# Performance work log

Measured on AMD Instinct MI355X. Metric: run time of the kernel, lower is better.

The kernel has to match this reference:

```python
import jax, jax.numpy as jnp
import numpy as np

N_NODES = 100000
N_EDGES = 1600000
IN_F = 67
H1, C1 = 10, 8   # heads, per-head channels layer 1
H2, C2 = 1, 1    # layer 2


def setup_inputs() -> dict:
    key = jax.random.key(0)
    ks = jax.random.split(key, 10)
    x = jax.random.normal(ks[0], (N_NODES, IN_F), dtype=jnp.float32)
    edge_index = jax.random.randint(ks[1], (2, N_EDGES), 0, N_NODES, dtype=jnp.int64)
    s = 0.1
    W1 = jax.random.normal(ks[2], (IN_F, H1 * C1), dtype=jnp.float32) * s
    att_src1 = jax.random.normal(ks[3], (H1, C1), dtype=jnp.float32) * s
    att_dst1 = jax.random.normal(ks[4], (H1, C1), dtype=jnp.float32) * s
    b1 = jnp.zeros((H1 * C1,), dtype=jnp.float32)
    W2 = jax.random.normal(ks[5], (H1 * C1, H2 * C2), dtype=jnp.float32) * s
    att_src2 = jax.random.normal(ks[6], (H2, C2), dtype=jnp.float32) * s
    att_dst2 = jax.random.normal(ks[7], (H2, C2), dtype=jnp.float32) * s
    b2 = jnp.zeros((H2 * C2,), dtype=jnp.float32)
    return {"x": x, "edge_index": edge_index, "W1": W1, "att_src1": att_src1,
            "att_dst1": att_dst1, "b1": b1, "W2": W2, "att_src2": att_src2,
            "att_dst2": att_dst2, "b2": b2}


def gat_conv(x, src, dst, W, att_src, att_dst, bias, heads, out_ch):
    """PyG GATConv (eval mode): gather -> leaky_relu -> segment softmax -> scatter."""
    n = x.shape[0]
    h = (x @ W).reshape(n, heads, out_ch)                     # [N,H,C]
    a_src = jnp.sum(h * att_src, axis=-1)                     # [N,H]
    a_dst = jnp.sum(h * att_dst, axis=-1)                     # [N,H]
    e = a_src[src] + a_dst[dst]                               # [E,H]
    e = jax.nn.leaky_relu(e, negative_slope=0.2)
    # numerically stable softmax over edges grouped by destination node
    m = jax.ops.segment_max(e, dst, num_segments=n)           # [N,H]
    ex = jnp.exp(e - m[dst])
    denom = jax.ops.segment_sum(ex, dst, num_segments=n)      # [N,H]
    alpha = ex / denom[dst]                                   # [E,H]
    msg = h[src] * alpha[:, :, None]                          # [E,H,C]
    out = jax.ops.segment_sum(msg, dst, num_segments=n)       # [N,H,C]
    return out.reshape(n, heads * out_ch) + bias


def reference(x, edge_index, W1, att_src1, att_dst1, b1, W2, att_src2, att_dst2, b2):
    n = x.shape[0]
    loops = jnp.arange(n, dtype=edge_index.dtype)
    src = jnp.concatenate([edge_index[0], loops])             # add_self_loops=True
    dst = jnp.concatenate([edge_index[1], loops])
    h = gat_conv(x, src, dst, W1, att_src1, att_dst1, b1, H1, C1)
    h = jax.nn.elu(h)
    out = gat_conv(h, src, dst, W2, att_src2, att_dst2, b2, H2, C2)
    return out
```

## Files before the change

### kernel.cpp

```cpp
#include <hip/hip_runtime.h>
#include <math.h>

#define IN_F 67
#define F1   80
#define NH1  10
#define NC1  8

#define GN   64
#define KS   104
#define PKS  96

#define CB    512
#define CSH   9
#define NBC   196
#define RB    64
#define NGRP  8
#define GCAP  1536
#define SLCAP 1664
#define CSTRIDE 16
#define NFB   512
#define CHUNK 2048
#define A2T   4

typedef _Float16 h16;
typedef h16 h16x2 __attribute__((ext_vector_type(2)));
typedef h16 h16x8 __attribute__((ext_vector_type(8)));
typedef float f32x4 __attribute__((ext_vector_type(4)));
typedef float f32x4u __attribute__((ext_vector_type(4), aligned(4)));
typedef int i32x4 __attribute__((ext_vector_type(4)));

__global__ __launch_bounds__(256)
void k_front(const float* __restrict__ x, const float* __restrict__ W,
             const float* __restrict__ att_s, const float* __restrict__ att_d,
             const int* __restrict__ ei, int* __restrict__ gcur,
             int* __restrict__ ebuf, h16* __restrict__ pk,
             float* __restrict__ a_dst, int N, int E) {
    __shared__ __align__(16) char smem[GN * 81 * 4];
    const int tid = threadIdx.x;

    if ((int)blockIdx.x < NFB) {
        int2* sStage = (int2*)smem;
        int*  sCnt   = (int*)(smem + CHUNK * 8);
        int*  sGBase = sCnt + NBC;
        int*  sScan  = sGBase + NBC;
        int*  wsum   = sScan + 256;
        const int g = blockIdx.x & (NGRP - 1);
        const int lane = tid & 63;
        const int wv = tid >> 6;

        for (int base_e = blockIdx.x * CHUNK; base_e < E; base_e += NFB * CHUNK) {
            int lim = E - base_e; if (lim > CHUNK) lim = CHUNK;
            for (int i = tid; i < NBC; i += 256) sCnt[i] = 0;
            __syncthreads();

            int2 ev[8]; int pos[8]; int nloc = 0;
            int e0 = base_e + tid * 8;
            if (tid * 8 + 8 <= lim) {
                i32x4 s0 = *(const i32x4*)(ei + e0);
                i32x4 s1 = *(const i32x4*)(ei + e0 + 4);
                i32x4 d0 = *(const i32x4*)(ei + E + e0);
                i32x4 d1 = *(const i32x4*)(ei + E + e0 + 4);
#pragma unroll
                for (int j = 0; j < 4; ++j) { ev[j] = make_int2(s0[j], d0[j]); }
#pragma unroll
                for (int j = 0; j < 4; ++j) { ev[4 + j] = make_int2(s1[j], d1[j]); }
                nloc = 8;
            } else {
                for (int j = 0; j < 8; ++j) {
                    int e = e0 + j;
                    if (tid * 8 + j < lim) { ev[nloc++] = make_int2(ei[e], ei[E + e]); }
                }
            }
            for (int j = 0; j < nloc; ++j)
                pos[j] = atomicAdd(&sCnt[ev[j].y >> CSH], 1);
            __syncthreads();

            int v = (tid < NBC) ? sCnt[tid] : 0;
            int sc = v;
#pragma unroll
            for (int o = 1; o < 64; o <<= 1) {
                int u = __shfl_up(sc, o);
                if (lane >= o) sc += u;
            }
            if (lane == 63) wsum[wv] = sc;
            __syncthreads();
            int add = 0;
#pragma unroll
            for (int w = 0; w < 4; ++w) add += (w < wv) ? wsum[w] : 0;
            sScan[tid] = sc + add;
            if (tid < NBC && v > 0)
                sGBase[tid] = atomicAdd(&gcur[((size_t)g * NBC + tid) * CSTRIDE], v);
            __syncthreads();

            for (int j = 0; j < nloc; ++j) {
                int B = ev[j].y >> CSH;
                sStage[sScan[B] - sCnt[B] + pos[j]] = ev[j];
            }
            __syncthreads();

            int total = sScan[NBC - 1];
            for (int i = tid; i < total; i += 256) {
                int2 e = sStage[i];
                int B = e.y >> CSH;
                int gp = sGBase[B] + (i - (sScan[B] - sCnt[B]));
                if (gp < GCAP)
                    ebuf[((size_t)g * NBC + B) * GCAP + gp] = e.x | ((e.y & (CB - 1)) << 17);
            }
            __syncthreads();
        }
        return;
    }

    h16*   sWt = (h16*)smem;
    float* sO  = (float*)smem;
    const int node0 = (blockIdx.x - NFB) * GN;

    if (tid < 240) {
        int c = tid - (tid >= 160 ? 160 : (tid >= 80 ? 80 : 0));
        int kb = (tid >= 160 ? 64 : (tid >= 80 ? 32 : 0));
        h16 tmp[32];
#pragma unroll
        for (int j = 0; j < 32; ++j) {
            int k = kb + j;
            tmp[j] = (h16)((k < IN_F) ? W[k * F1 + c] : 0.f);
        }
        h16* dst = sWt + c * KS + kb;
#pragma unroll
        for (int j = 0; j < 4; ++j)
            *(h16x8*)(dst + j * 8) = *(const h16x8*)(tmp + j * 8);
    }
    __syncthreads();

    const int lane = tid & 63;
    const int m    = lane & 15;
    const int quad = lane >> 4;
    const int wn0  = (tid >> 6) * 16;

    int gn  = node0 + wn0 + m;
    int gnc = gn < N ? gn : N - 1;
    const float* xr = x + (size_t)gnc * IN_F;

    f32x4 acc[5];
#pragma unroll
    for (int ct = 0; ct < 5; ++ct) acc[ct] = (f32x4){0.f, 0.f, 0.f, 0.f};

#pragma unroll
    for (int ks = 0; ks < 64; ks += 32) {
        int k0 = ks + quad * 8;
        f32x4 a0 = *(const f32x4u*)(xr + k0);
        f32x4 a1 = *(const f32x4u*)(xr + k0 + 4);
        h16x8 af;
        af[0] = (h16)a0.x; af[1] = (h16)a0.y; af[2] = (h16)a0.z; af[3] = (h16)a0.w;
        af[4] = (h16)a1.x; af[5] = (h16)a1.y; af[6] = (h16)a1.z; af[7] = (h16)a1.w;
#pragma unroll
        for (int ct = 0; ct < 5; ++ct) {
            h16x8 bf = *(const h16x8*)(sWt + (ct * 16 + m) * KS + ks + quad * 8);
            acc[ct] = __builtin_amdgcn_mfma_f32_16x16x32_f16(af, bf, acc[ct], 0, 0, 0);
        }
    }
    {
        h16x8 af = (h16x8)(h16)0.f;
        if (quad == 0) {
            af[0] = (h16)xr[64]; af[1] = (h16)xr[65]; af[2] = (h16)xr[66];
        }
#pragma unroll
        for (int ct = 0; ct < 5; ++ct) {
            h16x8 bf = *(const h16x8*)(sWt + (ct * 16 + m) * KS + 64 + quad * 8);
            acc[ct] = __builtin_amdgcn_mfma_f32_16x16x32_f16(af, bf, acc[ct], 0, 0, 0);
        }
    }
    __syncthreads();

#pragma unroll
    for (int ct = 0; ct < 5; ++ct)
#pragma unroll
        for (int r = 0; r < 4; ++r)
            sO[(wn0 + quad * 4 + r) * 81 + ct * 16 + m] = acc[ct][r];
    __syncthreads();

    for (int idx = tid; idx < GN * (F1 / 2); idx += 256) {
        int n = idx / (F1 / 2);
        int p = idx - n * (F1 / 2);
        int gg = node0 + n;
        if (gg < N) {
            h16x2 v;
            v.x = (h16)sO[n * 81 + 2 * p];
            v.y = (h16)sO[n * 81 + 2 * p + 1];
            *(h16x2*)(pk + (size_t)gg * PKS + 2 * p) = v;
        }
    }
    for (int t = tid; t < GN * NH1; t += 256) {
        int n = t / NH1;
        int h = t - n * NH1;
        int gg = node0 + n;
        if (gg < N) {
            const float* hr = sO + n * 81 + h * NC1;
            float s = 0.f, d = 0.f;
#pragma unroll
            for (int c = 0; c < NC1; ++c) {
                float v = hr[c];
                s += v * att_s[h * NC1 + c];
                d += v * att_d[h * NC1 + c];
            }
            pk[(size_t)gg * PKS + F1 + h] = (h16)s;
            a_dst[gg * NH1 + h] = d;
        }
    }
}

__global__ __launch_bounds__(256)
void k_agg1(const int* __restrict__ ebuf, const int* __restrict__ gcur,
            const h16* __restrict__ pk, const float* __restrict__ a_dst,
            const float* __restrict__ b1, const float* __restrict__ W2,
            const float* __restrict__ att_s2, const float* __restrict__ att_d2,
            float2* __restrict__ hs2, float* __restrict__ a_dst2,
            int* __restrict__ row, int* __restrict__ deg, int* __restrict__ csr2,
            int N, int NB) {
    __shared__ int   sTmp[SLCAP];
    __shared__ int   sList[SLCAP];
    __shared__ int   s_cnt[RB];
    __shared__ int   s_scan[RB];
    __shared__ int   s_cur[RB];
    __shared__ float s_acc[RB];
    __shared__ int   sTot;

    const int tid = threadIdx.x;
    const int lane = tid & 63;
    const int b = blockIdx.x;
    const int B = b >> 3;
    const int q = b & 7;
    const int lo = b * RB;

    for (int i = tid; i < RB; i += 256) { s_cnt[i] = 1; s_acc[i] = 0.f; }
    if (tid == 0) sTot = 0;
    __syncthreads();

    for (int g = 0; g < NGRP; ++g) {
        size_t slot = (size_t)g * NBC + B;
        int cnt = gcur[slot * CSTRIDE];
        cnt = cnt < GCAP ? cnt : GCAP;
        const int* eb = ebuf + slot * GCAP;
        for (int i0 = 0; i0 < cnt; i0 += 256) {
            int i = i0 + tid;
            int v = 0, n_l = 0;
            bool match = false;
            if (i < cnt) {
                v = eb[i];
                int dloc = v >> 17;
                match = (dloc >> 6) == q;
                n_l = dloc & (RB - 1);
            }
            unsigned long long mk = __ballot(match);
            int base = 0;
            if (lane == 0 && mk) base = atomicAdd(&sTot, __popcll(mk));
            base = __shfl(base, 0);
            if (match) {
                atomicAdd(&s_cnt[n_l], 1);
                int p = base + __popcll(mk & ((1ull << lane) - 1));
                if (p < SLCAP) sTmp[p] = (v & 0x1FFFF) | (n_l << 17);
            }
        }
    }
    __syncthreads();

    if (tid < RB) {
        int cntv = s_cnt[tid];
        int sc = cntv;
#pragma unroll
        for (int o = 1; o < RB; o <<= 1) {
            int u = __shfl_up(sc, o);
            if (tid >= o) sc += u;
        }
        s_scan[tid] = sc;
        int excl = sc - cntv;
        int n = lo + tid;
        if (excl < SLCAP) sList[excl] = n;
        s_cur[tid] = excl + 1;
        if (n < N) {
            int dg = cntv;
            if (excl + dg > SLCAP) dg = SLCAP - excl > 0 ? SLCAP - excl : 0;
            row[n] = b * SLCAP + excl;
            deg[n] = dg;
        }
    }
    __syncthreads();

    int total = sTot < SLCAP ? sTot : SLCAP;
    for (int i = tid; i < total; i += 256) {
        int u = sTmp[i];
        int n_l = u >> 17;
        int p = atomicAdd(&s_cur[n_l], 1);
        if (p < SLCAP) sList[p] = u & 0x1FFFF;
    }
    __syncthreads();

    int tot2 = s_scan[RB - 1];
    tot2 = tot2 < SLCAP ? tot2 : SLCAP;
    for (int i = tid; i < tot2; i += 256)
        csr2[(size_t)b * SLCAP + i] = sList[i];

    for (int t = tid; t < RB * NH1; t += 256) {
        int n_l = t / NH1;
        int h = t - n_l * NH1;
        int n = lo + n_l;
        if (n >= N) continue;
        int beg = s_scan[n_l] - s_cnt[n_l];
        int end = beg + s_cnt[n_l];
        end = end < SLCAP ? end : SLCAP;
        float ad = a_dst[n * NH1 + h];
        float den = 0.f;
        float num[NC1];
#pragma unroll
        for (int c = 0; c < NC1; ++c) num[c] = 0.f;

        int i = beg;
        for (; i + 3 < end; i += 4) {
            int sv[4];
#pragma unroll
            for (int j = 0; j < 4; ++j) sv[j] = sList[i + j];
            h16x8 qf[4];
            float a[4];
#pragma unroll
            for (int j = 0; j < 4; ++j) {
                const h16* rp = pk + (size_t)sv[j] * PKS;
                qf[j] = *(const h16x8*)(rp + h * NC1);
                a[j] = (float)rp[F1 + h];
            }
#pragma unroll
            for (int j = 0; j < 4; ++j) {
                float v = a[j] + ad;
                v = v > 0.f ? v : 0.2f * v;
                float w = __expf(v);
                den += w;
#pragma unroll
                for (int c = 0; c < NC1; ++c) num[c] += w * (float)qf[j][c];
            }
        }
        for (; i < end; ++i) {
            const h16* rp = pk + (size_t)sList[i] * PKS;
            h16x8 qf = *(const h16x8*)(rp + h * NC1);
            float v = (float)rp[F1 + h] + ad;
            v = v > 0.f ? v : 0.2f * v;
            float w = __expf(v);
            den += w;
#pragma unroll
            for (int c = 0; c < NC1; ++c) num[c] += w * (float)qf[c];
        }
        float inv = 1.f / den;
        const float* bb = b1 + h * NC1;
        const float* w2 = W2 + h * NC1;
        float p = 0.f;
#pragma unroll
        for (int c = 0; c < NC1; ++c) {
            float o = num[c] * inv + bb[c];
            o = o > 0.f ? o : expm1f(o);
            p += o * w2[c];
        }
        atomicAdd(&s_acc[n_l], p);
    }
    __syncthreads();

    if (tid < RB) {
        int n = lo + tid;
        if (n < N) {
            float acc = s_acc[tid];
            float2 v;
            v.x = acc;
            v.y = acc * att_s2[0];
            hs2[n] = v;
            a_dst2[n] = acc * att_d2[0];
        }
    }
}

__global__ __launch_bounds__(256)
void k_agg2(const int* __restrict__ row, const int* __restrict__ deg,
            const int* __restrict__ csr2, const float2* __restrict__ hs2,
            const float* __restrict__ a_dst2, const float* __restrict__ b2,
            float* __restrict__ out, int N) {
    int t = blockIdx.x * blockDim.x + threadIdx.x;
    int n = t >> 2;
    int sl = t & (A2T - 1);
    if (n >= N) return;
    float ad = a_dst2[n];
    int beg = row[n];
    int dg  = deg[n];
    float den = 0.f, num = 0.f;
    int i = sl;
    for (; i + A2T < dg; i += 2 * A2T) {
        int s0 = csr2[beg + i];
        int s1 = csr2[beg + i + A2T];
        float2 g0 = hs2[s0];
        float2 g1 = hs2[s1];
        float v0 = g0.y + ad; v0 = v0 > 0.f ? v0 : 0.2f * v0;
        float v1 = g1.y + ad; v1 = v1 > 0.f ? v1 : 0.2f * v1;
        float w0 = __expf(v0), w1 = __expf(v1);
        den += w0 + w1;
        num += w0 * g0.x + w1 * g1.x;
    }
    for (; i < dg; i += A2T) {
        float2 g = hs2[csr2[beg + i]];
        float v = g.y + ad;
        v = v > 0.f ? v : 0.2f * v;
        float w = __expf(v);
        den += w;
        num += w * g.x;
    }
    den += __shfl_xor(den, 1); num += __shfl_xor(num, 1);
    den += __shfl_xor(den, 2); num += __shfl_xor(num, 2);
    if (sl == 0) out[n] = num / den + b2[0];
}

extern "C" void kernel_launch(void* const* d_in, const int* in_sizes, int n_in,
                              void* d_out, int out_size, void* d_ws, size_t ws_size,
                              hipStream_t stream) {
    const float* x        = (const float*)d_in[0];
    const int*   ei       = (const int*)d_in[1];
    const float* W1       = (const float*)d_in[2];
    const float* att_src1 = (const float*)d_in[3];
    const float* att_dst1 = (const float*)d_in[4];
    const float* b1       = (const float*)d_in[5];
    const float* W2       = (const float*)d_in[6];
    const float* att_src2 = (const float*)d_in[7];
    const float* att_dst2 = (const float*)d_in[8];
    const float* b2       = (const float*)d_in[9];
    float* out = (float*)d_out;

    const int N  = in_sizes[0] / IN_F;
    const int E  = in_sizes[1] / 2;
    const int NB = (N + RB - 1) / RB;

    float*  ws      = (float*)d_ws;
    h16*    pk      = (h16*)ws;
    float*  a_dst1  = ws + (size_t)N * (PKS / 2);
    float2* hs2     = (float2*)(a_dst1 + (size_t)N * NH1);
    float*  a_dst2  = (float*)(hs2 + N);
    int*    row     = (int*)(a_dst2 + N);
    int*    deg     = row + N;
    int*    gcur    = deg + N;
    int*    csr2    = gcur + (size_t)NGRP * NBC * CSTRIDE;
    int*    ebuf    = csr2 + (size_t)NB * SLCAP;

    const int B = 256;
    const int nbG = (N + GN - 1) / GN;

    hipMemsetAsync(gcur, 0, (size_t)NGRP * NBC * CSTRIDE * sizeof(int), stream);
    k_front<<<NFB + nbG, 256, 0, stream>>>(x, W1, att_src1, att_dst1, ei,
                                           gcur, ebuf, pk, a_dst1, N, E);

    k_agg1<<<NB, 256, 0, stream>>>(ebuf, gcur, pk, a_dst1, b1, W2,
                                   att_src2, att_dst2, hs2, a_dst2,
                                   row, deg, csr2, N, NB);

    k_agg2<<<((size_t)N * A2T + B - 1) / B, B, 0, stream>>>(row, deg, csr2, hs2,
                                                            a_dst2, b2, out, N);
}
```

Measured before the change: 216.3 us.

## Stage gathered neighbor rows in shared memory for cooperative layer-1 aggregation

The layer-1 aggregation now copies neighbor feature rows from global memory into a shared-memory window, WEDGE edges at a time, using coalesced 16-byte loads across the whole block. Each thread holds up to three (node, head) accumulators in registers and reads the rows from LDS. Before, each head-thread did its own scattered global gather of the same row. This cuts redundant global traffic, since the ten heads of a node share one row. The cost is about 24KB of extra LDS, barriers per window, and a launch-bounds hint. Together these may lower occupancy or cause register spilling.

```diff
diff --git a/kernel.cpp b/kernel.cpp
--- a/kernel.cpp
+++ b/kernel.cpp
@@ -21,6 +21,8 @@
 #define NFB   512
 #define CHUNK 2048
 #define A2T   4
+#define WEDGE 128
+#define NSLOT 3
 
 typedef _Float16 h16;
 typedef h16 h16x2 __attribute__((ext_vector_type(2)));
@@ -208,7 +210,7 @@
     }
 }
 
-__global__ __launch_bounds__(256)
+__global__ __launch_bounds__(256, 4)
 void k_agg1(const int* __restrict__ ebuf, const int* __restrict__ gcur,
             const h16* __restrict__ pk, const float* __restrict__ a_dst,
             const float* __restrict__ b1, const float* __restrict__ W2,
@@ -218,6 +220,7 @@
             int N, int NB) {
     __shared__ int   sTmp[SLCAP];
     __shared__ int   sList[SLCAP];
+    __shared__ __align__(16) h16 sRow[WEDGE * PKS];
     __shared__ int   s_cnt[RB];
     __shared__ int   s_scan[RB];
     __shared__ int   s_cur[RB];
@@ -299,64 +302,79 @@
     for (int i = tid; i < tot2; i += 256)
         csr2[(size_t)b * SLCAP + i] = sList[i];
 
-    for (int t = tid; t < RB * NH1; t += 256) {
-        int n_l = t / NH1;
-        int h = t - n_l * NH1;
-        int n = lo + n_l;
-        if (n >= N) continue;
-        int beg = s_scan[n_l] - s_cnt[n_l];
-        int end = beg + s_cnt[n_l];
-        end = end < SLCAP ? end : SLCAP;
-        float ad = a_dst[n * NH1 + h];
-        float den = 0.f;
-        float num[NC1];
-#pragma unroll
-        for (int c = 0; c < NC1; ++c) num[c] = 0.f;
-
-        int i = beg;
-        for (; i + 3 < end; i += 4) {
-            int sv[4];
-#pragma unroll
-            for (int j = 0; j < 4; ++j) sv[j] = sList[i + j];
-            h16x8 qf[4];
-            float a[4];
-#pragma unroll
-            for (int j = 0; j < 4; ++j) {
-                const h16* rp = pk + (size_t)sv[j] * PKS;
-                qf[j] = *(const h16x8*)(rp + h * NC1);
-                a[j] = (float)rp[F1 + h];
-            }
-#pragma unroll
-            for (int j = 0; j < 4; ++j) {
-                float v = a[j] + ad;
+    int   begA[NSLOT], endA[NSLOT], hA[NSLOT], nlA[NSLOT];
+    float adA[NSLOT];
+    float den[NSLOT];
+    float num[NSLOT][NC1];
+#pragma unroll
+    for (int k = 0; k < NSLOT; ++k) {
+        int t = tid + k * 256;
+        begA[k] = 0; endA[k] = 0; hA[k] = 0; nlA[k] = 0; adA[k] = 0.f;
+        den[k] = 0.f;
+#pragma unroll
+        for (int c = 0; c < NC1; ++c) num[k][c] = 0.f;
+        if (t < RB * NH1) {
+            int n_l = t / NH1;
+            int h = t - n_l * NH1;
+            int n = lo + n_l;
+            nlA[k] = n_l; hA[k] = h;
+            if (n < N) {
+                int beg = s_scan[n_l] - s_cnt[n_l];
+                int end = beg + s_cnt[n_l];
+                end = end < tot2 ? end : tot2;
+                begA[k] = beg; endA[k] = end;
+                adA[k] = a_dst[n * NH1 + h];
+            }
+        }
+    }
+
+    for (int w0 = 0; w0 < tot2; w0 += WEDGE) {
+        int w1 = w0 + WEDGE; w1 = w1 < tot2 ? w1 : tot2;
+        __syncthreads();
+        int nchunk = (w1 - w0) * (PKS / 8);
+        for (int i = tid; i < nchunk; i += 256) {
+            int e = i / 12;
+            int c = i - e * 12;
+            *(h16x8*)(sRow + e * PKS + c * 8) =
+                *(const h16x8*)(pk + (size_t)sList[w0 + e] * PKS + c * 8);
+        }
+        __syncthreads();
+#pragma unroll
+        for (int k = 0; k < NSLOT; ++k) {
+            int lo_ = begA[k] > w0 ? begA[k] : w0;
+            int hi_ = endA[k] < w1 ? endA[k] : w1;
+            int h = hA[k];
+            float ad = adA[k];
+            for (int i = lo_; i < hi_; ++i) {
+                const h16* rp = sRow + (i - w0) * PKS;
+                h16x8 qf = *(const h16x8*)(rp + h * NC1);
+                float v = (float)rp[F1 + h] + ad;
                 v = v > 0.f ? v : 0.2f * v;
                 float w = __expf(v);
-                den += w;
-#pragma unroll
-                for (int c = 0; c < NC1; ++c) num[c] += w * (float)qf[j][c];
-            }
-        }
-        for (; i < end; ++i) {
-            const h16* rp = pk + (size_t)sList[i] * PKS;
-            h16x8 qf = *(const h16x8*)(rp + h * NC1);
-            float v = (float)rp[F1 + h] + ad;
-            v = v > 0.f ? v : 0.2f * v;
-            float w = __expf(v);
-            den += w;
-#pragma unroll
-            for (int c = 0; c < NC1; ++c) num[c] += w * (float)qf[c];
-        }
-        float inv = 1.f / den;
-        const float* bb = b1 + h * NC1;
-        const float* w2 = W2 + h * NC1;
-        float p = 0.f;
-#pragma unroll
-        for (int c = 0; c < NC1; ++c) {
-            float o = num[c] * inv + bb[c];
-            o = o > 0.f ? o : expm1f(o);
-            p += o * w2[c];
-        }
-        atomicAdd(&s_acc[n_l], p);
+                den[k] += w;
+#pragma unroll
+                for (int c = 0; c < NC1; ++c) num[k][c] += w * (float)qf[c];
+            }
+        }
+    }
+
+#pragma unroll
+    for (int k = 0; k < NSLOT; ++k) {
+        int t = tid + k * 256;
+        if (t < RB * NH1 && endA[k] > begA[k]) {
+            int h = hA[k];
+            float inv = 1.f / den[k];
+            const float* bb = b1 + h * NC1;
+            const float* w2 = W2 + h * NC1;
+            float p = 0.f;
+#pragma unroll
+            for (int c = 0; c < NC1; ++c) {
+                float o = num[k][c] * inv + bb[c];
+                o = o > 0.f ? o : expm1f(o);
+                p += o * w2[c];
+            }
+            atomicAdd(&s_acc[nlA[k]], p);
+        }
     }
     __syncthreads();
 
```

New measurement: 279.9 us. +29.4%, slower.

## Split layer-1 aggregation by head halves and combine via atomics

Applied to the files above, without the earlier changes.

Layer-1 features are stored as two packed half-tables of five heads each, and k_agg1 runs twice as many blocks, each handling one head half for a 64-node range. The two halves' partial layer-2 projections are combined with global atomicAdd into a zeroed buffer, and k_agg2 derives the attention scalars from that buffer itself. The edge-bucketing part of k_front now uses one chunk per block with more blocks instead of a strided loop. The intent is more parallelism and smaller gather rows, at the cost of each agg1 block redoing the bucket scan and list build, plus extra atomics.

```diff
diff --git a/kernel.cpp b/kernel.cpp
--- a/kernel.cpp
+++ b/kernel.cpp
@@ -5,10 +5,11 @@
 #define F1   80
 #define NH1  10
 #define NC1  8
+#define NHH  5
 
 #define GN   64
 #define KS   104
-#define PKS  96
+#define PKS_H 48
 
 #define CB    512
 #define CSH   9
@@ -18,7 +19,7 @@
 #define GCAP  1536
 #define SLCAP 1664
 #define CSTRIDE 16
-#define NFB   512
+#define NFB   782
 #define CHUNK 2048
 #define A2T   4
 
@@ -33,7 +34,7 @@
 void k_front(const float* __restrict__ x, const float* __restrict__ W,
              const float* __restrict__ att_s, const float* __restrict__ att_d,
              const int* __restrict__ ei, int* __restrict__ gcur,
-             int* __restrict__ ebuf, h16* __restrict__ pk,
+             int* __restrict__ ebuf, h16* __restrict__ pk0, h16* __restrict__ pk1,
              float* __restrict__ a_dst, int N, int E) {
     __shared__ __align__(16) char smem[GN * 81 * 4];
     const int tid = threadIdx.x;
@@ -48,7 +49,8 @@
         const int lane = tid & 63;
         const int wv = tid >> 6;
 
-        for (int base_e = blockIdx.x * CHUNK; base_e < E; base_e += NFB * CHUNK) {
+        int base_e = blockIdx.x * CHUNK;
+        if (base_e < E) {
             int lim = E - base_e; if (lim > CHUNK) lim = CHUNK;
             for (int i = tid; i < NBC; i += 256) sCnt[i] = 0;
             __syncthreads();
@@ -106,7 +108,6 @@
                 if (gp < GCAP)
                     ebuf[((size_t)g * NBC + B) * GCAP + gp] = e.x | ((e.y & (CB - 1)) << 17);
             }
-            __syncthreads();
         }
         return;
     }
@@ -178,31 +179,25 @@
             sO[(wn0 + quad * 4 + r) * 81 + ct * 16 + m] = acc[ct][r];
     __syncthreads();
 
-    for (int idx = tid; idx < GN * (F1 / 2); idx += 256) {
-        int n = idx / (F1 / 2);
-        int p = idx - n * (F1 / 2);
-        int gg = node0 + n;
-        if (gg < N) {
-            h16x2 v;
-            v.x = (h16)sO[n * 81 + 2 * p];
-            v.y = (h16)sO[n * 81 + 2 * p + 1];
-            *(h16x2*)(pk + (size_t)gg * PKS + 2 * p) = v;
-        }
-    }
     for (int t = tid; t < GN * NH1; t += 256) {
         int n = t / NH1;
         int h = t - n * NH1;
         int gg = node0 + n;
         if (gg < N) {
             const float* hr = sO + n * 81 + h * NC1;
+            h16x8 vf;
             float s = 0.f, d = 0.f;
 #pragma unroll
             for (int c = 0; c < NC1; ++c) {
                 float v = hr[c];
+                vf[c] = (h16)v;
                 s += v * att_s[h * NC1 + c];
                 d += v * att_d[h * NC1 + c];
             }
-            pk[(size_t)gg * PKS + F1 + h] = (h16)s;
+            int hl = h < NHH ? h : h - NHH;
+            h16* base = (h < NHH ? pk0 : pk1) + (size_t)gg * PKS_H;
+            *(h16x8*)(base + hl * 8) = vf;
+            base[NHH * NC1 + hl] = (h16)s;
             a_dst[gg * NH1 + h] = d;
         }
     }
@@ -210,10 +205,10 @@
 
 __global__ __launch_bounds__(256)
 void k_agg1(const int* __restrict__ ebuf, const int* __restrict__ gcur,
-            const h16* __restrict__ pk, const float* __restrict__ a_dst,
+            const h16* __restrict__ pk0, const h16* __restrict__ pk1,
+            const float* __restrict__ a_dst,
             const float* __restrict__ b1, const float* __restrict__ W2,
-            const float* __restrict__ att_s2, const float* __restrict__ att_d2,
-            float2* __restrict__ hs2, float* __restrict__ a_dst2,
+            float* __restrict__ hl2acc,
             int* __restrict__ row, int* __restrict__ deg, int* __restrict__ csr2,
             int N, int NB) {
     __shared__ int   sTmp[SLCAP];
@@ -226,7 +221,9 @@
 
     const int tid = threadIdx.x;
     const int lane = tid & 63;
-    const int b = blockIdx.x;
+    const int bb = blockIdx.x;
+    const int half = bb & 1;
+    const int b = bb >> 1;
     const int B = b >> 3;
     const int q = b & 7;
     const int lo = b * RB;
@@ -276,7 +273,7 @@
         int n = lo + tid;
         if (excl < SLCAP) sList[excl] = n;
         s_cur[tid] = excl + 1;
-        if (n < N) {
+        if (half == 0 && n < N) {
             int dg = cntv;
             if (excl + dg > SLCAP) dg = SLCAP - excl > 0 ? SLCAP - excl : 0;
             row[n] = b * SLCAP + excl;
@@ -296,18 +293,22 @@
 
     int tot2 = s_scan[RB - 1];
     tot2 = tot2 < SLCAP ? tot2 : SLCAP;
-    for (int i = tid; i < tot2; i += 256)
-        csr2[(size_t)b * SLCAP + i] = sList[i];
-
-    for (int t = tid; t < RB * NH1; t += 256) {
-        int n_l = t / NH1;
-        int h = t - n_l * NH1;
+    if (half == 0) {
+        for (int i = tid; i < tot2; i += 256)
+            csr2[(size_t)b * SLCAP + i] = sList[i];
+    }
+
+    const h16* pkh = half ? pk1 : pk0;
+    for (int t = tid; t < RB * NHH; t += 256) {
+        int n_l = t / NHH;
+        int h = t - n_l * NHH;
         int n = lo + n_l;
         if (n >= N) continue;
+        int hg = half * NHH + h;
         int beg = s_scan[n_l] - s_cnt[n_l];
         int end = beg + s_cnt[n_l];
         end = end < SLCAP ? end : SLCAP;
-        float ad = a_dst[n * NH1 + h];
+        float ad = a_dst[n * NH1 + hg];
         float den = 0.f;
         float num[NC1];
 #pragma unroll
@@ -322,9 +323,9 @@
             float a[4];
 #pragma unroll
             for (int j = 0; j < 4; ++j) {
-                const h16* rp = pk + (size_t)sv[j] * PKS;
+                const h16* rp = pkh + (size_t)sv[j] * PKS_H;
                 qf[j] = *(const h16x8*)(rp + h * NC1);
-                a[j] = (float)rp[F1 + h];
+                a[j] = (float)rp[NHH * NC1 + h];
             }
 #pragma unroll
             for (int j = 0; j < 4; ++j) {
@@ -337,9 +338,9 @@
             }
         }
         for (; i < end; ++i) {
-            const h16* rp = pk + (size_t)sList[i] * PKS;
+            const h16* rp = pkh + (size_t)sList[i] * PKS_H;
             h16x8 qf = *(const h16x8*)(rp + h * NC1);
-            float v = (float)rp[F1 + h] + ad;
+            float v = (float)rp[NHH * NC1 + h] + ad;
             v = v > 0.f ? v : 0.2f * v;
             float w = __expf(v);
             den += w;
@@ -347,12 +348,12 @@
             for (int c = 0; c < NC1; ++c) num[c] += w * (float)qf[c];
         }
         float inv = 1.f / den;
-        const float* bb = b1 + h * NC1;
-        const float* w2 = W2 + h * NC1;
+        const float* bb1 = b1 + hg * NC1;
+        const float* w2 = W2 + hg * NC1;
         float p = 0.f;
 #pragma unroll
         for (int c = 0; c < NC1; ++c) {
-            float o = num[c] * inv + bb[c];
+            float o = num[c] * inv + bb1[c];
             o = o > 0.f ? o : expm1f(o);
             p += o * w2[c];
         }
@@ -362,27 +363,21 @@
 
     if (tid < RB) {
         int n = lo + tid;
-        if (n < N) {
-            float acc = s_acc[tid];
-            float2 v;
-            v.x = acc;
-            v.y = acc * att_s2[0];
-            hs2[n] = v;
-            a_dst2[n] = acc * att_d2[0];
-        }
+        if (n < N) atomicAdd(&hl2acc[n], s_acc[tid]);
     }
 }
 
 __global__ __launch_bounds__(256)
 void k_agg2(const int* __restrict__ row, const int* __restrict__ deg,
-            const int* __restrict__ csr2, const float2* __restrict__ hs2,
-            const float* __restrict__ a_dst2, const float* __restrict__ b2,
-            float* __restrict__ out, int N) {
+            const int* __restrict__ csr2, const float* __restrict__ hl2acc,
+            const float* __restrict__ att_s2, const float* __restrict__ att_d2,
+            const float* __restrict__ b2, float* __restrict__ out, int N) {
     int t = blockIdx.x * blockDim.x + threadIdx.x;
     int n = t >> 2;
     int sl = t & (A2T - 1);
     if (n >= N) return;
-    float ad = a_dst2[n];
+    float as2 = att_s2[0];
+    float ad = hl2acc[n] * att_d2[0];
     int beg = row[n];
     int dg  = deg[n];
     float den = 0.f, num = 0.f;
@@ -390,21 +385,21 @@
     for (; i + A2T < dg; i += 2 * A2T) {
         int s0 = csr2[beg + i];
         int s1 = csr2[beg + i + A2T];
-        float2 g0 = hs2[s0];
-        float2 g1 = hs2[s1];
-        float v0 = g0.y + ad; v0 = v0 > 0.f ? v0 : 0.2f * v0;
-        float v1 = g1.y + ad; v1 = v1 > 0.f ? v1 : 0.2f * v1;
+        float g0 = hl2acc[s0];
+        float g1 = hl2acc[s1];
+        float v0 = g0 * as2 + ad; v0 = v0 > 0.f ? v0 : 0.2f * v0;
+        float v1 = g1 * as2 + ad; v1 = v1 > 0.f ? v1 : 0.2f * v1;
         float w0 = __expf(v0), w1 = __expf(v1);
         den += w0 + w1;
-        num += w0 * g0.x + w1 * g1.x;
+        num += w0 * g0 + w1 * g1;
     }
     for (; i < dg; i += A2T) {
-        float2 g = hs2[csr2[beg + i]];
-        float v = g.y + ad;
+        float g = hl2acc[csr2[beg + i]];
+        float v = g * as2 + ad;
         v = v > 0.f ? v : 0.2f * v;
         float w = __expf(v);
         den += w;
-        num += w * g.x;
+        num += w * g;
     }
     den += __shfl_xor(den, 1); num += __shfl_xor(num, 1);
     den += __shfl_xor(den, 2); num += __shfl_xor(num, 2);
@@ -431,27 +426,28 @@
     const int NB = (N + RB - 1) / RB;
 
     float*  ws      = (float*)d_ws;
-    h16*    pk      = (h16*)ws;
-    float*  a_dst1  = ws + (size_t)N * (PKS / 2);
-    float2* hs2     = (float2*)(a_dst1 + (size_t)N * NH1);
-    float*  a_dst2  = (float*)(hs2 + N);
-    int*    row     = (int*)(a_dst2 + N);
+    h16*    pk0     = (h16*)ws;
+    h16*    pk1     = pk0 + (size_t)N * PKS_H;
+    float*  a_dst1  = ws + (size_t)N * (2 * PKS_H / 2);
+    int*    row     = (int*)(a_dst1 + (size_t)N * NH1);
     int*    deg     = row + N;
-    int*    gcur    = deg + N;
+    float*  hl2acc  = (float*)(deg + N);
+    int*    gcur    = (int*)(hl2acc + N);
     int*    csr2    = gcur + (size_t)NGRP * NBC * CSTRIDE;
     int*    ebuf    = csr2 + (size_t)NB * SLCAP;
 
     const int B = 256;
     const int nbG = (N + GN - 1) / GN;
 
-    hipMemsetAsync(gcur, 0, (size_t)NGRP * NBC * CSTRIDE * sizeof(int), stream);
+    hipMemsetAsync(hl2acc, 0,
+                   ((size_t)N + (size_t)NGRP * NBC * CSTRIDE) * sizeof(int), stream);
     k_front<<<NFB + nbG, 256, 0, stream>>>(x, W1, att_src1, att_dst1, ei,
-                                           gcur, ebuf, pk, a_dst1, N, E);
-
-    k_agg1<<<NB, 256, 0, stream>>>(ebuf, gcur, pk, a_dst1, b1, W2,
-                                   att_src2, att_dst2, hs2, a_dst2,
-                                   row, deg, csr2, N, NB);
-
-    k_agg2<<<((size_t)N * A2T + B - 1) / B, B, 0, stream>>>(row, deg, csr2, hs2,
-                                                            a_dst2, b2, out, N);
+                                           gcur, ebuf, pk0, pk1, a_dst1, N, E);
+
+    k_agg1<<<2 * NB, 256, 0, stream>>>(ebuf, gcur, pk0, pk1, a_dst1, b1, W2,
+                                       hl2acc, row, deg, csr2, N, NB);
+
+    k_agg2<<<((size_t)N * A2T + B - 1) / B, B, 0, stream>>>(row, deg, csr2, hl2acc,
+                                                            att_src2, att_dst2, b2,
+                                                            out, N);
 }
```

After: 257.6 us. 19.1% more time.
